# Performance work log

Measured on AMD Instinct MI355X. Metric: run time of the kernel, lower is better.

## Reference

```python
import jax, jax.numpy as jnp
import numpy as np

N_RAYS = 262144
N_BINS = 127  # num_steps - 1 midpoints


def setup_inputs() -> dict:
    key = jax.random.key(0)
    kb, kw = jax.random.split(key)
    # bins are sorted z-midpoints along each ray: strictly increasing via cumsum
    db = jax.random.uniform(kb, (N_RAYS, N_BINS), dtype=jnp.float32) + 0.01
    bins = 0.2 + jnp.cumsum(db, axis=-1) * (3.8 / N_BINS)  # roughly [near, far]
    weights = jax.random.uniform(kw, (N_RAYS, N_BINS - 1), dtype=jnp.float32)
    return {"bins": bins, "weights": weights, "n_samples": 128}


def reference(bins, weights, n_samples):
    # sample_pdf with det=True (inference path: det = not self.training)
    weights = weights + 1e-5                       # [N, M]
    pdf = weights / jnp.sum(weights, -1, keepdims=True)
    cdf = jnp.cumsum(pdf, -1)
    cdf = jnp.concatenate([jnp.zeros_like(cdf[..., :1]), cdf], -1)  # [N, M+1]
    n = n_samples
    u = jnp.linspace(0.5 / n, 1.0 - 0.5 / n, n, dtype=cdf.dtype)
    u = jnp.broadcast_to(u, cdf.shape[:-1] + (n,))  # [N, S]

    # batched binary search: inds = #{cdf <= u} (right=True)
    inds = jax.vmap(lambda c, uu: jnp.searchsorted(c, uu, side="right"))(cdf, u)
    below = jnp.maximum(inds - 1, 0)
    above = jnp.minimum(inds, cdf.shape[-1] - 1)

    cdf_b = jnp.take_along_axis(cdf, below, axis=-1)
    cdf_a = jnp.take_along_axis(cdf, above, axis=-1)
    bins_b = jnp.take_along_axis(bins, below, axis=-1)
    bins_a = jnp.take_along_axis(bins, above, axis=-1)

    denom = cdf_a - cdf_b
    denom = jnp.where(denom < 1e-5, jnp.ones_like(denom), denom)
    t = (u - cdf_b) / denom
    samples = bins_b + t * (bins_a - bins_b)       # [N, S]
    return samples
```

## Files before the change

kernel.cpp:

```cpp
#include <hip/hip_runtime.h>


#define M     126
#define NBINS 127
#define NS    128
#define RPW   3
#define SEGW  130

template<int CTRL, int RM>
__device__ __forceinline__ float dpp_f(float x) {
    return __builtin_bit_cast(float,
        __builtin_amdgcn_update_dpp(0, __builtin_bit_cast(int, x),
                                    CTRL, RM, 0xf, true));
}
template<int CTRL, int RM>
__device__ __forceinline__ int dpp_i(int x) {
    return __builtin_amdgcn_update_dpp(0, x, CTRL, RM, 0xf, true);
}

__device__ __forceinline__ float wave_iscan_add(float x) {
    x += dpp_f<0x111, 0xf>(x);
    x += dpp_f<0x112, 0xf>(x);
    x += dpp_f<0x114, 0xf>(x);
    x += dpp_f<0x118, 0xf>(x);
    x += dpp_f<0x142, 0xa>(x);
    x += dpp_f<0x143, 0xc>(x);
    return x;
}
__device__ __forceinline__ int wave_iscan_max(int x) {
    x = max(x, dpp_i<0x111, 0xf>(x));
    x = max(x, dpp_i<0x112, 0xf>(x));
    x = max(x, dpp_i<0x114, 0xf>(x));
    x = max(x, dpp_i<0x118, 0xf>(x));
    x = max(x, dpp_i<0x142, 0xa>(x));
    x = max(x, dpp_i<0x143, 0xc>(x));
    return x;
}

__global__ __launch_bounds__(256) void sample_pdf_rank13(
    const float* __restrict__ bins,
    const float* __restrict__ weights,
    float* __restrict__ out,
    int n_rays)
{
    __shared__ int    s_idx[4 * RPW][SEGW];
    __shared__ float4 s_P[4 * RPW][NS / 2];

    const int wave = threadIdx.x >> 6;
    const int lane = threadIdx.x & 63;
    const int base = (blockIdx.x * 4 + wave) * RPW;

    const int i0 = min(2 * lane, 126);
    const int i1 = min(2 * lane + 1, 126);
    const int iw = min(2 * lane, 124);

    #pragma unroll
    for (int r = 0; r < RPW; ++r)
        *reinterpret_cast<int2*>(&s_idx[wave * RPW + r][2 * lane]) = make_int2(0, 0);

    float  b_a[RPW], b_b[RPW];
    float2 ww[RPW];
    #pragma unroll
    for (int r = 0; r < RPW; ++r) {
        const int ryu = min(base + r, n_rays - 1);
        const float* brow = bins    + (size_t)ryu * NBINS;
        const float* wrow = weights + (size_t)ryu * M;
        b_a[r] = brow[i0];
        b_b[r] = brow[i1];
        ww[r]  = *reinterpret_cast<const float2*>(wrow + iw);
    }
    __builtin_amdgcn_wave_barrier();

    const float u0 = fmaf((float)lane, 0.015625f, 0.00390625f);
    const float u1 = u0 + 0.0078125f;

    #pragma unroll
    for (int r = 0; r < RPW; ++r) {
        const float w0  = ww[r].x + 1e-5f;
        const float w1  = ww[r].y + 1e-5f;
        const float rw0 = __builtin_amdgcn_rcpf(w0);
        const float rw1 = __builtin_amdgcn_rcpf(w1);
        const float b_c = dpp_f<0x130, 0xf>(b_a[r]);

        const float pair  = w0 + w1;
        const float ps    = wave_iscan_add(pair);
        const float total = __shfl(ps, 62, 64);
        const float inv   = __builtin_amdgcn_rcpf(total);
        const float excl  = ps - pair;
        const float c0 = excl * inv;
        const float c1 = (excl + w0) * inv;
        const float c2 = ps * inv;

        const int g0 = (int)ceilf(fmaf(c0, 128.0f, -0.5f));
        const int g1 = (int)ceilf(fmaf(c1, 128.0f, -0.5f));

        const float dA = c1 - c0;
        const float dB = c2 - c1;
        const float fA = (dA < 1e-5f) ? 1.0f : total * rw0;
        const float fB = (dB < 1e-5f) ? 1.0f : total * rw1;
        const float slA = (b_b[r] - b_a[r]) * fA;
        const float slB = (b_c    - b_b[r]) * fB;
        const float A0  = fmaf(-c0, slA, b_a[r]);
        const float A1  = fmaf(-c1, slB, b_b[r]);

        const int seg = wave * RPW + r;
        s_P[seg][lane] = make_float4(A0, slA, A1, slB);
        atomicMax(&s_idx[seg][min(g0, 128)], 2 * lane);
        atomicMax(&s_idx[seg][min(g1, 128)], 2 * lane + 1);
    }
    __builtin_amdgcn_wave_barrier();

    #pragma unroll
    for (int r = 0; r < RPW; ++r) {
        const int seg = wave * RPW + r;
        const int2 xi = *reinterpret_cast<const int2*>(&s_idx[seg][2 * lane]);
        const int  m  = wave_iscan_max(max(xi.x, xi.y));
        const int  e  = dpp_i<0x138, 0xf>(m);
        const int  K0 = max(e, xi.x);
        const int  K1 = max(K0, xi.y);

        const float2* P = reinterpret_cast<const float2*>(&s_P[seg][0]);
        const float2 p0 = P[K0];
        const float2 p1 = P[K1];
        float2 res;
        res.x = fmaf(u0, p0.y, p0.x);
        res.y = fmaf(u1, p1.y, p1.x);
        if (base + r < n_rays) {
            *reinterpret_cast<float2*>(out + (size_t)(base + r) * NS + 2 * lane) = res;
        }
    }
}

extern "C" void kernel_launch(void* const* d_in, const int* in_sizes, int n_in,
                              void* d_out, int out_size, void* d_ws, size_t ws_size,
                              hipStream_t stream) {
    const float* bins    = (const float*)d_in[0];
    const float* weights = (const float*)d_in[1];
    float* out = (float*)d_out;

    const int n_rays = in_sizes[0] / NBINS;
    const int rays_per_block = 4 * RPW;
    const int blocks = (n_rays + rays_per_block - 1) / rays_per_block;
    sample_pdf_rank13<<<blocks, 256, 0, stream>>>(bins, weights, out, n_rays);
}
```

Before: 75.12 us.

## Convert sample_pdf kernel to persistent grid-stride loop with fixed block count

Launches a fixed grid of 2048 blocks, each looping over rays with a grid stride, instead of one block per twelve rays. Shared index buffers are re-zeroed after each iteration. The inclusive scan now masks lane 63 to zero and reads the total from lane 63, and out-of-range indices are skipped instead of clamped into padding. The aim is to cut block launch and scheduling overhead. The cost is less latency hiding, because each wave's loads are not overlapped across iterations.

After: 81.03 us. 7.9% more time.

```diff
diff --git a/kernel.cpp b/kernel.cpp
--- a/kernel.cpp
+++ b/kernel.cpp
@@ -5,7 +5,7 @@
 #define NBINS 127
 #define NS    128
 #define RPW   3
-#define SEGW  130
+#define NBLK  2048
 
 template<int CTRL, int RM>
 __device__ __forceinline__ float dpp_f(float x) {
@@ -37,97 +37,107 @@
     return x;
 }
 
-__global__ __launch_bounds__(256) void sample_pdf_rank13(
+__global__ __launch_bounds__(256) void sample_pdf_persist(
     const float* __restrict__ bins,
     const float* __restrict__ weights,
     float* __restrict__ out,
     int n_rays)
 {
-    __shared__ int    s_idx[4 * RPW][SEGW];
+    __shared__ int    s_idx[4 * RPW][NS];
     __shared__ float4 s_P[4 * RPW][NS / 2];
 
-    const int wave = threadIdx.x >> 6;
+    const int tid  = __builtin_amdgcn_readfirstlane(threadIdx.x);
+    const int wave = tid >> 6;
     const int lane = threadIdx.x & 63;
-    const int base = (blockIdx.x * 4 + wave) * RPW;
+    const int segbase = wave * RPW;
+    const int stride  = NBLK * 4 * RPW;
 
     const int i0 = min(2 * lane, 126);
     const int i1 = min(2 * lane + 1, 126);
     const int iw = min(2 * lane, 124);
-
-    #pragma unroll
-    for (int r = 0; r < RPW; ++r)
-        *reinterpret_cast<int2*>(&s_idx[wave * RPW + r][2 * lane]) = make_int2(0, 0);
-
-    float  b_a[RPW], b_b[RPW];
-    float2 ww[RPW];
-    #pragma unroll
-    for (int r = 0; r < RPW; ++r) {
-        const int ryu = min(base + r, n_rays - 1);
-        const float* brow = bins    + (size_t)ryu * NBINS;
-        const float* wrow = weights + (size_t)ryu * M;
-        b_a[r] = brow[i0];
-        b_b[r] = brow[i1];
-        ww[r]  = *reinterpret_cast<const float2*>(wrow + iw);
-    }
-    __builtin_amdgcn_wave_barrier();
-
+    const bool full = (lane < 63);
     const float u0 = fmaf((float)lane, 0.015625f, 0.00390625f);
     const float u1 = u0 + 0.0078125f;
 
     #pragma unroll
-    for (int r = 0; r < RPW; ++r) {
-        const float w0  = ww[r].x + 1e-5f;
-        const float w1  = ww[r].y + 1e-5f;
-        const float rw0 = __builtin_amdgcn_rcpf(w0);
-        const float rw1 = __builtin_amdgcn_rcpf(w1);
-        const float b_c = dpp_f<0x130, 0xf>(b_a[r]);
-
-        const float pair  = w0 + w1;
-        const float ps    = wave_iscan_add(pair);
-        const float total = __shfl(ps, 62, 64);
-        const float inv   = __builtin_amdgcn_rcpf(total);
-        const float excl  = ps - pair;
-        const float c0 = excl * inv;
-        const float c1 = (excl + w0) * inv;
-        const float c2 = ps * inv;
-
-        const int g0 = (int)ceilf(fmaf(c0, 128.0f, -0.5f));
-        const int g1 = (int)ceilf(fmaf(c1, 128.0f, -0.5f));
-
-        const float dA = c1 - c0;
-        const float dB = c2 - c1;
-        const float fA = (dA < 1e-5f) ? 1.0f : total * rw0;
-        const float fB = (dB < 1e-5f) ? 1.0f : total * rw1;
-        const float slA = (b_b[r] - b_a[r]) * fA;
-        const float slB = (b_c    - b_b[r]) * fB;
-        const float A0  = fmaf(-c0, slA, b_a[r]);
-        const float A1  = fmaf(-c1, slB, b_b[r]);
-
-        const int seg = wave * RPW + r;
-        s_P[seg][lane] = make_float4(A0, slA, A1, slB);
-        atomicMax(&s_idx[seg][min(g0, 128)], 2 * lane);
-        atomicMax(&s_idx[seg][min(g1, 128)], 2 * lane + 1);
-    }
+    for (int r = 0; r < RPW; ++r)
+        *reinterpret_cast<int2*>(&s_idx[segbase + r][2 * lane]) = make_int2(0, 0);
     __builtin_amdgcn_wave_barrier();
 
-    #pragma unroll
-    for (int r = 0; r < RPW; ++r) {
-        const int seg = wave * RPW + r;
-        const int2 xi = *reinterpret_cast<const int2*>(&s_idx[seg][2 * lane]);
-        const int  m  = wave_iscan_max(max(xi.x, xi.y));
-        const int  e  = dpp_i<0x138, 0xf>(m);
-        const int  K0 = max(e, xi.x);
-        const int  K1 = max(K0, xi.y);
+    for (int base = (blockIdx.x * 4 + wave) * RPW; base < n_rays; base += stride) {
 
-        const float2* P = reinterpret_cast<const float2*>(&s_P[seg][0]);
-        const float2 p0 = P[K0];
-        const float2 p1 = P[K1];
-        float2 res;
-        res.x = fmaf(u0, p0.y, p0.x);
-        res.y = fmaf(u1, p1.y, p1.x);
-        if (base + r < n_rays) {
-            *reinterpret_cast<float2*>(out + (size_t)(base + r) * NS + 2 * lane) = res;
+        float  b_a[RPW], b_b[RPW];
+        float2 ww[RPW];
+        #pragma unroll
+        for (int r = 0; r < RPW; ++r) {
+            const int ryu = min(base + r, n_rays - 1);
+            const float* brow = bins    + (size_t)ryu * NBINS;
+            const float* wrow = weights + (size_t)ryu * M;
+            b_a[r] = brow[i0];
+            b_b[r] = brow[i1];
+            ww[r]  = *reinterpret_cast<const float2*>(wrow + iw);
         }
+
+        #pragma unroll
+        for (int r = 0; r < RPW; ++r) {
+            const float w0  = full ? ww[r].x + 1e-5f : 0.0f;
+            const float w1  = full ? ww[r].y + 1e-5f : 0.0f;
+            const float rw0 = __builtin_amdgcn_rcpf(w0);
+            const float rw1 = __builtin_amdgcn_rcpf(w1);
+            const float b_c = dpp_f<0x130, 0xf>(b_a[r]);
+
+            const float pair  = w0 + w1;
+            const float ps    = wave_iscan_add(pair);
+            const float total = __shfl(ps, 63, 64);
+            const float inv   = __builtin_amdgcn_rcpf(total);
+            const float excl  = ps - pair;
+            const float c0 = excl * inv;
+            const float c1 = (excl + w0) * inv;
+            const float c2 = ps * inv;
+
+            const int g0 = (int)ceilf(fmaf(c0, 128.0f, -0.5f));
+            const int g1 = (int)ceilf(fmaf(c1, 128.0f, -0.5f));
+
+            const float dA = c1 - c0;
+            const float dB = c2 - c1;
+            const float fA = (dA < 1e-5f) ? 1.0f : total * rw0;
+            const float fB = (dB < 1e-5f) ? 1.0f : total * rw1;
+            const float slA = (b_b[r] - b_a[r]) * fA;
+            const float slB = (b_c    - b_b[r]) * fB;
+            const float A0  = fmaf(-c0, slA, b_a[r]);
+            const float A1  = fmaf(-c1, slB, b_b[r]);
+
+            const int seg = segbase + r;
+            s_P[seg][lane] = make_float4(A0, slA, A1, slB);
+            if (g0 < NS) atomicMax(&s_idx[seg][g0], 2 * lane);
+            if (g1 < NS) atomicMax(&s_idx[seg][g1], 2 * lane + 1);
+        }
+        __builtin_amdgcn_wave_barrier();
+
+        #pragma unroll
+        for (int r = 0; r < RPW; ++r) {
+            const int seg = segbase + r;
+            const int2 xi = *reinterpret_cast<const int2*>(&s_idx[seg][2 * lane]);
+            const int  m  = wave_iscan_max(max(xi.x, xi.y));
+            const int  e  = dpp_i<0x138, 0xf>(m);
+            const int  K0 = max(e, xi.x);
+            const int  K1 = max(K0, xi.y);
+
+            const float2* P = reinterpret_cast<const float2*>(&s_P[seg][0]);
+            const float2 p0 = P[K0];
+            const float2 p1 = P[K1];
+            float2 res;
+            res.x = fmaf(u0, p0.y, p0.x);
+            res.y = fmaf(u1, p1.y, p1.x);
+            if (base + r < n_rays) {
+                *reinterpret_cast<float2*>(out + (size_t)(base + r) * NS + 2 * lane) = res;
+            }
+        }
+
+        #pragma unroll
+        for (int r = 0; r < RPW; ++r)
+            *reinterpret_cast<int2*>(&s_idx[segbase + r][2 * lane]) = make_int2(0, 0);
+        __builtin_amdgcn_wave_barrier();
     }
 }
 
@@ -139,7 +149,5 @@
     float* out = (float*)d_out;
 
     const int n_rays = in_sizes[0] / NBINS;
-    const int rays_per_block = 4 * RPW;
-    const int blocks = (n_rays + rays_per_block - 1) / rays_per_block;
-    sample_pdf_rank13<<<blocks, 256, 0, stream>>>(bins, weights, out, n_rays);
+    sample_pdf_persist<<<NBLK, 256, 0, stream>>>(bins, weights, out, n_rays);
 }
```
